# Optimization experiments

Measured on AMD Instinct MI355X. Metric: run time of the kernel, lower is better.

Reference implementation:

```python
import jax, jax.numpy as jnp
import numpy as np

K = 6  # knn_number
EPS_CS = 1e-8  # F.cosine_similarity eps


def _sqdist(a, b):
    # a: [B,N,3], b: [B,M,3] -> [B,N,M] squared euclidean distances
    return (jnp.sum(a * a, -1)[:, :, None]
            + jnp.sum(b * b, -1)[:, None, :]
            - 2.0 * jnp.einsum('bnc,bmc->bnm', a, b))


def _batch_norm(x):
    # normalize last dim with the module's exact epsilons
    n = jnp.sqrt(jnp.sum(x * x, axis=-1, keepdims=True) + 1e-08)
    return x / (n + 1e-10)


def _cossim(a, b):
    # torch F.cosine_similarity semantics along last dim
    na = jnp.maximum(jnp.sqrt(jnp.sum(a * a, -1)), EPS_CS)
    nb = jnp.maximum(jnp.sqrt(jnp.sum(b * b, -1)), EPS_CS)
    return jnp.sum(a * b, -1) / (na * nb)


def _gather(points, idx):
    # points: [B,N,C], idx: [B,...] int -> [B,...,C]
    return jax.vmap(lambda p, i: p[i])(points, idx)


def _avg_ori(group_ori, group_nor, batch_ori, batch_nor):
    # group_*: [B,N,K,3], batch_*: [B,N,3]
    nor_diff = jnp.sum(group_nor * batch_nor[:, :, None, :], axis=3)  # [B,N,K]
    nor_diff = jnp.exp(-nor_diff / 0.3) * 10.0 + 1.0
    nor_diff = jnp.where(nor_diff < 4.0, 1.0, 5.0)
    batch_ori_rot = jnp.cross(batch_ori, batch_nor)  # get_ori_rot90: ori x nor
    cos0 = _cossim(group_ori, batch_ori[:, :, None, :])       # [B,N,K]
    cos1 = _cossim(group_ori, batch_ori_rot[:, :, None, :])   # [B,N,K]
    cos = jnp.minimum(1.0 - jnp.abs(cos0), 1.0 - jnp.abs(cos1))
    return jnp.mean(nor_diff * cos)


def _forward(ori_pre, nor_pre, xyz_up, xyz_offset, pts, gt):
    ori_pre = _batch_norm(ori_pre)
    nor_pre = _batch_norm(nor_pre)
    xyz_gt = gt[:, :, 0:3]
    xyz_nor = gt[:, :, 3:6]

    # ori-loss: NN of pts in gt, gather gt normals
    index = jnp.argmin(_sqdist(pts, xyz_gt), axis=2)  # [B,N]
    nor_gt = _gather(xyz_nor, index)                  # [B,N,3]
    d_n = jnp.sum(nor_gt * ori_pre, axis=2, keepdims=True)
    ori_pro = _batch_norm(ori_pre - nor_gt * d_n)

    # smooth field over KNN (self-knn over pts, includes self)
    idx = jax.lax.top_k(-_sqdist(pts, pts), K)[1]  # [B,N,K]
    group_ori = _gather(ori_pro, idx)              # [B,N,K,3]
    group_nor = _gather(nor_gt, idx)
    loss_smooth = _avg_ori(group_ori, group_nor, ori_pro, nor_gt)

    # normal estimation loss
    loss_nor = jnp.mean(1.0 - jnp.abs(_cossim(nor_gt, nor_pre)))

    # chamfer distances (squared-dist chamfer)
    do = _sqdist(xyz_offset, xyz_gt)
    loss_charm_offset = jnp.mean(jnp.min(do, axis=2)) + jnp.mean(jnp.min(do, axis=1))
    du = _sqdist(xyz_up, xyz_gt)
    loss_charm = jnp.mean(jnp.min(du, axis=2)) + jnp.mean(jnp.min(du, axis=1))

    # nor-ori orthogonality
    loss_nor_ori = jnp.mean(jnp.abs(jnp.sum(ori_pre * nor_gt, axis=2)))

    loss_cd = loss_charm + 0.4 * loss_charm_offset
    loss = loss_smooth + loss_nor + 0.1 * loss_nor_ori + 200.0 * loss_cd
    return (loss, loss_smooth, loss_nor, loss_charm_offset, loss_nor_ori, loss_charm, loss_charm)


def setup_inputs() -> dict:
    key = jax.random.key(0)
    k = jax.random.split(key, 6)
    B, N, NG, NU = 4, 4096, 4096, 8192
    gt_xyz = jax.random.normal(k[5], (B, NG, 3), dtype=jnp.float32)
    gt_nor = _batch_norm(jax.random.normal(jax.random.fold_in(key, 7), (B, NG, 3), dtype=jnp.float32))
    return {
        'ori_pre': jax.random.normal(k[0], (B, N, 3), dtype=jnp.float32),
        'nor_pre': jax.random.normal(k[1], (B, N, 3), dtype=jnp.float32),
        'xyz_up': jax.random.normal(k[2], (B, NU, 3), dtype=jnp.float32),
        'xyz_offset': jax.random.normal(k[3], (B, NU, 3), dtype=jnp.float32),
        'pts': jax.random.normal(k[4], (B, N, 3), dtype=jnp.float32),
        'gt': jnp.concatenate([gt_xyz, gt_nor], axis=-1),
        'epoch': 1,
    }


def reference(ori_pre, nor_pre, xyz_up, xyz_offset, pts, gt, epoch):
    # epoch is unused by the original forward as well
    return _forward(ori_pre, nor_pre, xyz_up, xyz_offset, pts, gt)
```

## Files before the change

kernel.cpp:

```cpp
#include <hip/hip_runtime.h>
#include <stdint.h>

#define NN 4096
#define NGG 4096
#define NUU 8192

__device__ __forceinline__ unsigned fkey32(float f) {
  unsigned u = __float_as_uint(f);
  return u ^ (((int)u >> 31) | 0x80000000u);
}
__device__ __forceinline__ float unfkey32(unsigned k) {
  unsigned m = (k & 0x80000000u) ? 0x80000000u : 0xFFFFFFFFu;
  return __uint_as_float(k ^ m);
}

__device__ __forceinline__ float block_sum_256(float v, float* sbuf) {
#pragma unroll
  for (int o = 32; o > 0; o >>= 1) v += __shfl_down(v, o, 64);
  int lane = threadIdx.x & 63;
  int w = threadIdx.x >> 6;
  if (lane == 0) sbuf[w] = v;
  __syncthreads();
  float r = 0.f;
  if (threadIdx.x == 0) r = sbuf[0] + sbuf[1] + sbuf[2] + sbuf[3];
  __syncthreads();
  return r;
}

__device__ __forceinline__ float block_sum_512(float v, float* sbuf) {
#pragma unroll
  for (int o = 32; o > 0; o >>= 1) v += __shfl_down(v, o, 64);
  int lane = threadIdx.x & 63;
  int w = threadIdx.x >> 6;
  if (lane == 0) sbuf[w] = v;
  __syncthreads();
  float r = 0.f;
  if (threadIdx.x == 0) {
#pragma unroll
    for (int i = 0; i < 8; ++i) r += sbuf[i];
  }
  __syncthreads();
  return r;
}

__global__ __launch_bounds__(256) void k_scan(const float* __restrict__ pts,
                                              const float* __restrict__ gt,
                                              const float* __restrict__ up,
                                              const float* __restrict__ off,
                                              unsigned long long* __restrict__ keys,
                                              unsigned* __restrict__ rowmin,
                                              unsigned* __restrict__ colmin,
                                              float* __restrict__ acc) {
  __shared__ float4 sc[512];
  int blk = blockIdx.x;
  int tid = threadIdx.x;
  if (blk == 0 && tid < 16) acc[tid] = 0.f;

  if (blk < 512) {
    int qb = blk >> 3;
    int seg = blk & 7;
    int wb = qb >> 3;
    int which = wb >> 2;
    int b = wb & 3;
    int r0 = (qb & 7) * 1024 + tid * 4;
    {
      const float* gtb = gt + (size_t)b * NGG * 6 + (size_t)seg * 512 * 6;
      int i0 = tid * 2;
      const float4* g4 = (const float4*)(gtb + (size_t)i0 * 6);
      float4 u0 = g4[0], u1 = g4[1], u2 = g4[2];
      sc[i0] = make_float4(u0.x, u0.y, u0.z,
                           fmaf(u0.x, u0.x, fmaf(u0.y, u0.y, u0.z * u0.z)));
      sc[i0 + 1] = make_float4(u1.z, u1.w, u2.x,
                               fmaf(u1.z, u1.z, fmaf(u1.w, u1.w, u2.x * u2.x)));
    }
    const float* src = which ? up : off;
    const float4* s4 = (const float4*)src;
    size_t fb = ((size_t)(b * NUU + r0) * 3) >> 2;
    float4 A = s4[fb], B = s4[fb + 1], C = s4[fb + 2];
    float q0x = A.x, q0y = A.y, q0z = A.z;
    float q1x = A.w, q1y = B.x, q1z = B.y;
    float q2x = B.z, q2y = B.w, q2z = C.x;
    float q3x = C.y, q3y = C.z, q3z = C.w;
    float qq0 = fmaf(q0x, q0x, fmaf(q0y, q0y, q0z * q0z));
    float qq1 = fmaf(q1x, q1x, fmaf(q1y, q1y, q1z * q1z));
    float qq2 = fmaf(q2x, q2x, fmaf(q2y, q2y, q2z * q2z));
    float qq3 = fmaf(q3x, q3x, fmaf(q3y, q3y, q3z * q3z));
    float a0x = -2.f * q0x, a0y = -2.f * q0y, a0z = -2.f * q0z;
    float a1x = -2.f * q1x, a1y = -2.f * q1y, a1z = -2.f * q1z;
    float a2x = -2.f * q2x, a2y = -2.f * q2y, a2z = -2.f * q2z;
    float a3x = -2.f * q3x, a3y = -2.f * q3y, a3z = -2.f * q3z;
    __syncthreads();
    float b0 = 3.4e38f, b1 = 3.4e38f, b2 = 3.4e38f, b3 = 3.4e38f;
#pragma unroll 4
    for (int j = 0; j < 512; ++j) {
      float4 c = sc[j];
      float t;
      t = fmaf(c.x, a0x, c.w); t = fmaf(c.y, a0y, t); t = fmaf(c.z, a0z, t); b0 = fminf(b0, t);
      t = fmaf(c.x, a1x, c.w); t = fmaf(c.y, a1y, t); t = fmaf(c.z, a1z, t); b1 = fminf(b1, t);
      t = fmaf(c.x, a2x, c.w); t = fmaf(c.y, a2y, t); t = fmaf(c.z, a2z, t); b2 = fminf(b2, t);
      t = fmaf(c.x, a3x, c.w); t = fmaf(c.y, a3y, t); t = fmaf(c.z, a3z, t); b3 = fminf(b3, t);
    }
    int gr = which * 32768 + b * NUU + r0;
    atomicMin(&rowmin[gr + 0], fkey32(b0 + qq0));
    atomicMin(&rowmin[gr + 1], fkey32(b1 + qq1));
    atomicMin(&rowmin[gr + 2], fkey32(b2 + qq2));
    atomicMin(&rowmin[gr + 3], fkey32(b3 + qq3));

  } else if (blk < 1024) {
    int blk2 = blk - 512;
    int qb = blk2 >> 4;
    int seg = blk2 & 15;
    int which = qb >> 4;
    int b = (qb >> 2) & 3;
    int m0 = (qb & 3) * 1024 + tid * 4;
    const float* src = which ? up : off;
    if (tid < 128) {
      const float* sb = src + (size_t)b * NUU * 3 + (size_t)seg * 512 * 3;
      int i0 = tid * 4;
      const float4* s4 = (const float4*)(sb + (size_t)i0 * 3);
      float4 u0 = s4[0], u1 = s4[1], u2 = s4[2];
      sc[i0] = make_float4(u0.x, u0.y, u0.z,
                           fmaf(u0.x, u0.x, fmaf(u0.y, u0.y, u0.z * u0.z)));
      sc[i0 + 1] = make_float4(u0.w, u1.x, u1.y,
                               fmaf(u0.w, u0.w, fmaf(u1.x, u1.x, u1.y * u1.y)));
      sc[i0 + 2] = make_float4(u1.z, u1.w, u2.x,
                               fmaf(u1.z, u1.z, fmaf(u1.w, u1.w, u2.x * u2.x)));
      sc[i0 + 3] = make_float4(u2.y, u2.z, u2.w,
                               fmaf(u2.y, u2.y, fmaf(u2.z, u2.z, u2.w * u2.w)));
    }
    const float* g = gt + (size_t)b * NGG * 6 + (size_t)m0 * 6;
    float q0x = g[0],  q0y = g[1],  q0z = g[2];
    float q1x = g[6],  q1y = g[7],  q1z = g[8];
    float q2x = g[12], q2y = g[13], q2z = g[14];
    float q3x = g[18], q3y = g[19], q3z = g[20];
    float qq0 = fmaf(q0x, q0x, fmaf(q0y, q0y, q0z * q0z));
    float qq1 = fmaf(q1x, q1x, fmaf(q1y, q1y, q1z * q1z));
    float qq2 = fmaf(q2x, q2x, fmaf(q2y, q2y, q2z * q2z));
    float qq3 = fmaf(q3x, q3x, fmaf(q3y, q3y, q3z * q3z));
    float a0x = -2.f * q0x, a0y = -2.f * q0y, a0z = -2.f * q0z;
    float a1x = -2.f * q1x, a1y = -2.f * q1y, a1z = -2.f * q1z;
    float a2x = -2.f * q2x, a2y = -2.f * q2y, a2z = -2.f * q2z;
    float a3x = -2.f * q3x, a3y = -2.f * q3y, a3z = -2.f * q3z;
    __syncthreads();
    float b0 = 3.4e38f, b1 = 3.4e38f, b2 = 3.4e38f, b3 = 3.4e38f;
#pragma unroll 4
    for (int j = 0; j < 512; ++j) {
      float4 c = sc[j];
      float t;
      t = fmaf(c.x, a0x, c.w); t = fmaf(c.y, a0y, t); t = fmaf(c.z, a0z, t); b0 = fminf(b0, t);
      t = fmaf(c.x, a1x, c.w); t = fmaf(c.y, a1y, t); t = fmaf(c.z, a1z, t); b1 = fminf(b1, t);
      t = fmaf(c.x, a2x, c.w); t = fmaf(c.y, a2y, t); t = fmaf(c.z, a2z, t); b2 = fminf(b2, t);
      t = fmaf(c.x, a3x, c.w); t = fmaf(c.y, a3y, t); t = fmaf(c.z, a3z, t); b3 = fminf(b3, t);
    }
    int gc = which * 16384 + b * NGG + m0;
    atomicMin(&colmin[gc + 0], fkey32(b0 + qq0));
    atomicMin(&colmin[gc + 1], fkey32(b1 + qq1));
    atomicMin(&colmin[gc + 2], fkey32(b2 + qq2));
    atomicMin(&colmin[gc + 3], fkey32(b3 + qq3));

  } else {
    int blk3 = blk - 1024;
    int qb = blk3 >> 4;
    int seg = blk3 & 15;
    int b = qb >> 2;
    int m0 = (qb & 3) * 1024 + tid * 4;
    if (tid < 128) {
      const float* gtb = gt + (size_t)b * NGG * 6 + (size_t)seg * 256 * 6;
      int i0 = tid * 2;
      const float4* g4 = (const float4*)(gtb + (size_t)i0 * 6);
      float4 u0 = g4[0], u1 = g4[1], u2 = g4[2];
      sc[i0] = make_float4(u0.x, u0.y, u0.z,
                           fmaf(u0.x, u0.x, fmaf(u0.y, u0.y, u0.z * u0.z)));
      sc[i0 + 1] = make_float4(u1.z, u1.w, u2.x,
                               fmaf(u1.z, u1.z, fmaf(u1.w, u1.w, u2.x * u2.x)));
    }
    size_t fb = ((size_t)(b * NN + m0) * 3) >> 2;
    const float4* p4 = (const float4*)pts;
    float4 A = p4[fb], B = p4[fb + 1], C = p4[fb + 2];
    float q0x = A.x, q0y = A.y, q0z = A.z;
    float q1x = A.w, q1y = B.x, q1z = B.y;
    float q2x = B.z, q2y = B.w, q2z = C.x;
    float q3x = C.y, q3y = C.z, q3z = C.w;
    float a0x = -2.f * q0x, a0y = -2.f * q0y, a0z = -2.f * q0z;
    float a1x = -2.f * q1x, a1y = -2.f * q1y, a1z = -2.f * q1z;
    float a2x = -2.f * q2x, a2y = -2.f * q2y, a2z = -2.f * q2z;
    float a3x = -2.f * q3x, a3y = -2.f * q3y, a3z = -2.f * q3z;
    __syncthreads();
    float b0 = 3.4e38f, b1 = 3.4e38f, b2 = 3.4e38f, b3 = 3.4e38f;
    int i0 = 0, i1 = 0, i2 = 0, i3 = 0;
#pragma unroll 4
    for (int j = 0; j < 256; ++j) {
      float4 c = sc[j];
      float t; bool cc;
      t = fmaf(c.x, a0x, c.w); t = fmaf(c.y, a0y, t); t = fmaf(c.z, a0z, t);
      cc = t < b0; b0 = cc ? t : b0; i0 = cc ? j : i0;
      t = fmaf(c.x, a1x, c.w); t = fmaf(c.y, a1y, t); t = fmaf(c.z, a1z, t);
      cc = t < b1; b1 = cc ? t : b1; i1 = cc ? j : i1;
      t = fmaf(c.x, a2x, c.w); t = fmaf(c.y, a2y, t); t = fmaf(c.z, a2z, t);
      cc = t < b2; b2 = cc ? t : b2; i2 = cc ? j : i2;
      t = fmaf(c.x, a3x, c.w); t = fmaf(c.y, a3y, t); t = fmaf(c.z, a3z, t);
      cc = t < b3; b3 = cc ? t : b3; i3 = cc ? j : i3;
    }
    int q = b * NN + m0;
    int base = seg * 256;
    atomicMin(&keys[q + 0], ((unsigned long long)fkey32(b0) << 32) | (unsigned)(base + i0));
    atomicMin(&keys[q + 1], ((unsigned long long)fkey32(b1) << 32) | (unsigned)(base + i1));
    atomicMin(&keys[q + 2], ((unsigned long long)fkey32(b2) << 32) | (unsigned)(base + i2));
    atomicMin(&keys[q + 3], ((unsigned long long)fkey32(b3) << 32) | (unsigned)(base + i3));
  }
}

__global__ __launch_bounds__(256) void k_post(
    const float* __restrict__ ori_pre, const float* __restrict__ nor_pre,
    const float* __restrict__ gt, const unsigned long long* __restrict__ keys,
    const unsigned* __restrict__ rowmin, const unsigned* __restrict__ colmin,
    float* __restrict__ nor_gt, float* __restrict__ ori_pro, float* __restrict__ acc) {
  __shared__ float sb1[4], sb2[4];
  int blk = blockIdx.x;
  if (blk < 64) {
    int q = blk * 256 + threadIdx.x;
    int b = q >> 12;
    float ox = ori_pre[q * 3 + 0], oy = ori_pre[q * 3 + 1], oz = ori_pre[q * 3 + 2];
    float n1 = sqrtf(fmaf(ox, ox, fmaf(oy, oy, oz * oz)) + 1e-8f) + 1e-10f;
    ox /= n1; oy /= n1; oz /= n1;
    float px = nor_pre[q * 3 + 0], py = nor_pre[q * 3 + 1], pz = nor_pre[q * 3 + 2];
    float n2 = sqrtf(fmaf(px, px, fmaf(py, py, pz * pz)) + 1e-8f) + 1e-10f;
    px /= n2; py /= n2; pz /= n2;
    unsigned idx = (unsigned)(keys[q] & 0xffffffffULL);
    const float* g = gt + (size_t)b * NGG * 6 + (size_t)idx * 6 + 3;
    float gx = g[0], gy = g[1], gz = g[2];
    float dn = fmaf(gx, ox, fmaf(gy, oy, gz * oz));
    float vx = ox - gx * dn, vy = oy - gy * dn, vz = oz - gz * dn;
    float n3 = sqrtf(fmaf(vx, vx, fmaf(vy, vy, vz * vz)) + 1e-8f) + 1e-10f;
    vx /= n3; vy /= n3; vz /= n3;
    nor_gt[q * 3 + 0] = gx; nor_gt[q * 3 + 1] = gy; nor_gt[q * 3 + 2] = gz;
    ori_pro[q * 3 + 0] = vx; ori_pro[q * 3 + 1] = vy; ori_pro[q * 3 + 2] = vz;
    float na = fmaxf(sqrtf(fmaf(gx, gx, fmaf(gy, gy, gz * gz))), 1e-8f);
    float nb = fmaxf(sqrtf(fmaf(px, px, fmaf(py, py, pz * pz))), 1e-8f);
    float cs = fmaf(gx, px, fmaf(gy, py, gz * pz)) / (na * nb);
    float t_nor = 1.f - fabsf(cs);
    float t_ori = fabsf(dn);
    float s1 = block_sum_256(t_nor, sb1);
    float s2 = block_sum_256(t_ori, sb2);
    if (threadIdx.x == 0) {
      atomicAdd(&acc[1], s1);
      atomicAdd(&acc[2], s2);
    }
  } else {
    int rblk = blk - 64;
    float v;
    int slot;
    if (rblk < 256) {
      int i = rblk * 256 + threadIdx.x;
      v = unfkey32(rowmin[i]);
      slot = (i >> 15) ? 5 : 3;
    } else {
      int i = (rblk - 256) * 256 + threadIdx.x;
      v = unfkey32(colmin[i]);
      slot = (i >> 14) ? 6 : 4;
    }
    float s = block_sum_256(v, sb1);
    if (threadIdx.x == 0) atomicAdd(&acc[slot], s);
  }
}

#define EV(i, QX, QY, QZ) \
  fmaf(c##i##z, (QZ), fmaf(c##i##y, (QY), fmaf(c##i##x, (QX), c##i##w)))

#define MIN8Q(QX, QY, QZ) \
  fminf(fminf(fminf(EV(0, QX, QY, QZ), EV(1, QX, QY, QZ)),                    \
              fminf(EV(2, QX, QY, QZ), EV(3, QX, QY, QZ))),                   \
        fminf(fminf(EV(4, QX, QY, QZ), EV(5, QX, QY, QZ)),                    \
              fminf(EV(6, QX, QY, QZ), EV(7, QX, QY, QZ))))

#define WREDMIN(M)                                            \
  {                                                           \
    M = fminf(M, __shfl_xor(M, 32, 64));                      \
    M = fminf(M, __shfl_xor(M, 16, 64));                      \
    M = fminf(M, __shfl_xor(M, 8, 64));                       \
    M = fminf(M, __shfl_xor(M, 4, 64));                       \
    M = fminf(M, __shfl_xor(M, 2, 64));                       \
    M = fminf(M, __shfl_xor(M, 1, 64));                       \
  }

#define PUSH1(QI, E, IDX)                                                     \
  if ((E) <= tq) {                                                            \
    unsigned sl = atomicAdd(&scnt[QI], 1u);                                   \
    if (sl < 96)                                                              \
      surv[QI][sl] = ((unsigned long long)fkey32(E) << 32) | (unsigned)(IDX); \
  }

#define PASSB_Q(QI, QX, QY, QZ)                                               \
  {                                                                           \
    float tq = stau[QI];                                                      \
    float e0 = EV(0, QX, QY, QZ), e1 = EV(1, QX, QY, QZ);                     \
    float e2 = EV(2, QX, QY, QZ), e3 = EV(3, QX, QY, QZ);                     \
    float e4 = EV(4, QX, QY, QZ), e5 = EV(5, QX, QY, QZ);                     \
    float e6 = EV(6, QX, QY, QZ), e7 = EV(7, QX, QY, QZ);                     \
    float mm = fminf(fminf(fminf(e0, e1), fminf(e2, e3)),                     \
                     fminf(fminf(e4, e5), fminf(e6, e7)));                    \
    if (mm <= tq) {                                                           \
      int base = tid * 8;                                                     \
      PUSH1(QI, e0, base + 0) PUSH1(QI, e1, base + 1)                         \
      PUSH1(QI, e2, base + 2) PUSH1(QI, e3, base + 3)                         \
      PUSH1(QI, e4, base + 4) PUSH1(QI, e5, base + 5)                         \
      PUSH1(QI, e6, base + 6) PUSH1(QI, e7, base + 7)                         \
    }                                                                         \
  }

#define TAUC(VI)                                                              \
  {                                                                           \
    int nct = (v0 <= (VI)) + (v1 <= (VI)) + (v2 <= (VI)) + (v3 <= (VI)) +     \
              (v4 <= (VI)) + (v5 <= (VI)) + (v6 <= (VI)) + (v7 <= (VI));      \
    if (nct >= 6) tau = fminf(tau, (VI));                                     \
  }

__global__ __launch_bounds__(512, 4) void k_knn_smooth(const float* __restrict__ pts,
                                                       const float* __restrict__ nor_gt,
                                                       const float* __restrict__ ori_pro,
                                                       float* __restrict__ acc,
                                                       float* __restrict__ out) {
  __shared__ unsigned long long surv[16][96];
  __shared__ unsigned scnt[16];
  __shared__ float wmin[8][16];
  __shared__ float stau[16];
  __shared__ float sred[8];
  int tid = threadIdx.x;
  int lane = tid & 63;
  int wave = tid >> 6;
  int blk = blockIdx.x;
  int b = blk >> 8;
  const float* pb = pts + (size_t)b * NN * 3;
  const float* pq = pb + (size_t)((blk & 255) * 16) * 3;

  if (tid < 16) scnt[tid] = 0;

  float c0x, c0y, c0z, c0w, c1x, c1y, c1z, c1w, c2x, c2y, c2z, c2w,
      c3x, c3y, c3z, c3w, c4x, c4y, c4z, c4w, c5x, c5y, c5z, c5w,
      c6x, c6y, c6z, c6w, c7x, c7y, c7z, c7w;
  {
    const float4* p4 = (const float4*)(pb + (size_t)tid * 24);
    float4 u0 = p4[0], u1 = p4[1], u2 = p4[2], u3 = p4[3], u4 = p4[4], u5 = p4[5];
    c0x = u0.x; c0y = u0.y; c0z = u0.z;
    c1x = u0.w; c1y = u1.x; c1z = u1.y;
    c2x = u1.z; c2y = u1.w; c2z = u2.x;
    c3x = u2.y; c3y = u2.z; c3z = u2.w;
    c4x = u3.x; c4y = u3.y; c4z = u3.z;
    c5x = u3.w; c5y = u4.x; c5z = u4.y;
    c6x = u4.z; c6y = u4.w; c6z = u5.x;
    c7x = u5.y; c7y = u5.z; c7z = u5.w;
    c0w = fmaf(c0x, c0x, fmaf(c0y, c0y, c0z * c0z));
    c1w = fmaf(c1x, c1x, fmaf(c1y, c1y, c1z * c1z));
    c2w = fmaf(c2x, c2x, fmaf(c2y, c2y, c2z * c2z));
    c3w = fmaf(c3x, c3x, fmaf(c3y, c3y, c3z * c3z));
    c4w = fmaf(c4x, c4x, fmaf(c4y, c4y, c4z * c4z));
    c5w = fmaf(c5x, c5x, fmaf(c5y, c5y, c5z * c5z));
    c6w = fmaf(c6x, c6x, fmaf(c6y, c6y, c6z * c6z));
    c7w = fmaf(c7x, c7x, fmaf(c7y, c7y, c7z * c7z));
  }

  for (int ch = 0; ch < 4; ++ch) {
    const float* qp = pq + ch * 12;
    float Q0x = -2.f * qp[0],  Q0y = -2.f * qp[1],  Q0z = -2.f * qp[2];
    float Q1x = -2.f * qp[3],  Q1y = -2.f * qp[4],  Q1z = -2.f * qp[5];
    float Q2x = -2.f * qp[6],  Q2y = -2.f * qp[7],  Q2z = -2.f * qp[8];
    float Q3x = -2.f * qp[9],  Q3y = -2.f * qp[10], Q3z = -2.f * qp[11];
    float m0 = MIN8Q(Q0x, Q0y, Q0z);
    float m1 = MIN8Q(Q1x, Q1y, Q1z);
    float m2 = MIN8Q(Q2x, Q2y, Q2z);
    float m3 = MIN8Q(Q3x, Q3y, Q3z);
    WREDMIN(m0) WREDMIN(m1) WREDMIN(m2) WREDMIN(m3)
    if (lane == 0) {
      wmin[wave][ch * 4 + 0] = m0;
      wmin[wave][ch * 4 + 1] = m1;
      wmin[wave][ch * 4 + 2] = m2;
      wmin[wave][ch * 4 + 3] = m3;
    }
  }
  __syncthreads();

  if (tid < 16) {
    float v0 = wmin[0][tid], v1 = wmin[1][tid], v2 = wmin[2][tid],
          v3 = wmin[3][tid], v4 = wmin[4][tid], v5 = wmin[5][tid],
          v6 = wmin[6][tid], v7 = wmin[7][tid];
    float tau = 3.4e38f;
    TAUC(v0) TAUC(v1) TAUC(v2) TAUC(v3) TAUC(v4) TAUC(v5) TAUC(v6) TAUC(v7)
    stau[tid] = tau;
  }
  __syncthreads();

  for (int ch = 0; ch < 4; ++ch) {
    const float* qp = pq + ch * 12;
    float Q0x = -2.f * qp[0],  Q0y = -2.f * qp[1],  Q0z = -2.f * qp[2];
    float Q1x = -2.f * qp[3],  Q1y = -2.f * qp[4],  Q1z = -2.f * qp[5];
    float Q2x = -2.f * qp[6],  Q2y = -2.f * qp[7],  Q2z = -2.f * qp[8];
    float Q3x = -2.f * qp[9],  Q3y = -2.f * qp[10], Q3z = -2.f * qp[11];
    PASSB_Q(ch * 4 + 0, Q0x, Q0y, Q0z)
    PASSB_Q(ch * 4 + 1, Q1x, Q1y, Q1z)
    PASSB_Q(ch * 4 + 2, Q2x, Q2y, Q2z)
    PASSB_Q(ch * 4 + 3, Q3x, Q3y, Q3z)
  }
  __syncthreads();

  int q_local = tid >> 5;
  int t = tid & 31;
  int q = blk * 16 + q_local;
  unsigned cnt = scnt[q_local];
  if (cnt > 96) cnt = 96;
  unsigned long long l0 = ~0ULL, l1 = ~0ULL, l2 = ~0ULL;
  for (int i = t; i < (int)cnt; i += 32) {
    unsigned long long k = surv[q_local][i];
    bool cc; unsigned long long nk;
    cc = k < l0; nk = cc ? k : l0; k = cc ? l0 : k; l0 = nk;
    cc = k < l1; nk = cc ? k : l1; k = cc ? l1 : k; l1 = nk;
    cc = k < l2; nk = cc ? k : l2;                  l2 = nk;
  }
  int myid = 0;
#pragma unroll
  for (int r = 0; r < 6; ++r) {
    unsigned long long h = l0, mk = l0;
#pragma unroll
    for (int o = 16; o > 0; o >>= 1) {
      unsigned long long other = __shfl_xor(mk, o, 32);
      mk = (other < mk) ? other : mk;
    }
    if (t == r) myid = (int)(mk & 0xffffffffULL);
    if (h == mk) { l0 = l1; l1 = l2; l2 = ~0ULL; }
  }

  float sum = 0.f;
  if (t < 6) {
    const float* gq = nor_gt + (size_t)q * 3;
    float ngx = gq[0], ngy = gq[1], ngz = gq[2];
    const float* oq = ori_pro + (size_t)q * 3;
    float box = oq[0], boy = oq[1], boz = oq[2];
    float rx = boy * ngz - boz * ngy;
    float ry = boz * ngx - box * ngz;
    float rz = box * ngy - boy * ngx;
    float nbo = fmaxf(sqrtf(fmaf(box, box, fmaf(boy, boy, boz * boz))), 1e-8f);
    float nrot = fmaxf(sqrtf(fmaf(rx, rx, fmaf(ry, ry, rz * rz))), 1e-8f);
    const float* gn = nor_gt + (size_t)(b * 4096 + myid) * 3;
    const float* go = ori_pro + (size_t)(b * 4096 + myid) * 3;
    float gnx = gn[0], gny = gn[1], gnz = gn[2];
    float gox = go[0], goy = go[1], goz = go[2];
    float ndv = fmaf(gnx, ngx, fmaf(gny, ngy, gnz * ngz));
    float wv = (expf(-ndv / 0.3f) * 10.f + 1.f) < 4.f ? 1.f : 5.f;
    float ngo = fmaxf(sqrtf(fmaf(gox, gox, fmaf(goy, goy, goz * goz))), 1e-8f);
    float c0 = fmaf(gox, box, fmaf(goy, boy, goz * boz)) / (ngo * nbo);
    float c1 = fmaf(gox, rx, fmaf(goy, ry, goz * rz)) / (ngo * nrot);
    float cosv = fminf(1.f - fabsf(c0), 1.f - fabsf(c1));
    sum = wv * cosv;
  }
  float s = block_sum_512(sum, sred);

  if (tid == 0) {
    atomicAdd(&acc[0], s);
    __threadfence();
    unsigned c = atomicAdd((unsigned*)(acc + 9), 1u);
    if (c == gridDim.x - 1) {
      __threadfence();
      float a0 = atomicAdd(&acc[0], 0.f);
      float a1 = atomicAdd(&acc[1], 0.f);
      float a2 = atomicAdd(&acc[2], 0.f);
      float a3 = atomicAdd(&acc[3], 0.f);
      float a4 = atomicAdd(&acc[4], 0.f);
      float a5 = atomicAdd(&acc[5], 0.f);
      float a6 = atomicAdd(&acc[6], 0.f);
      float loss_smooth = a0 / 98304.f;
      float loss_nor = a1 / 16384.f;
      float loss_nor_ori = a2 / 16384.f;
      float lco = a3 / 32768.f + a4 / 16384.f;
      float lc = a5 / 32768.f + a6 / 16384.f;
      float loss_cd = lc + 0.4f * lco;
      float loss = loss_smooth + loss_nor + 0.1f * loss_nor_ori + 200.f * loss_cd;
      out[0] = loss;
      out[1] = loss_smooth;
      out[2] = loss_nor;
      out[3] = lco;
      out[4] = loss_nor_ori;
      out[5] = lc;
      out[6] = lc;
    }
  }
}

extern "C" void kernel_launch(void* const* d_in, const int* in_sizes, int n_in,
                              void* d_out, int out_size, void* d_ws, size_t ws_size,
                              hipStream_t stream) {
  (void)in_sizes; (void)n_in; (void)out_size; (void)ws_size;
  const float* ori_pre = (const float*)d_in[0];
  const float* nor_pre = (const float*)d_in[1];
  const float* xyz_up = (const float*)d_in[2];
  const float* xyz_off = (const float*)d_in[3];
  const float* pts = (const float*)d_in[4];
  const float* gt = (const float*)d_in[5];
  float* out = (float*)d_out;
  char* ws = (char*)d_ws;

  float* acc = (float*)(ws + 0);
  unsigned long long* keys = (unsigned long long*)(ws + 512);
  unsigned* rowmin = (unsigned*)(ws + 512 + 131072);
  unsigned* colmin = (unsigned*)(ws + 512 + 131072 + 262144);
  float* nor_gt = (float*)(ws + 512 + 131072 + 262144 + 131072);
  float* ori_pro = (float*)(ws + 512 + 131072 + 262144 + 131072 + 196608);

  hipMemsetAsync(ws + 512, 0xFF, 131072 + 262144 + 131072, stream);

  k_scan<<<1280, 256, 0, stream>>>(pts, gt, xyz_up, xyz_off, keys, rowmin,
                                   colmin, acc);
  k_post<<<448, 256, 0, stream>>>(ori_pre, nor_pre, gt, keys, rowmin, colmin,
                                  nor_gt, ori_pro, acc);
  k_knn_smooth<<<1024, 512, 0, stream>>>(pts, nor_gt, ori_pro, acc, out);
}
```

Baseline: 170.5 us.

## Fuse post-processing kernel into KNN smooth kernel, recomputing projected orientations on the fly

Removes the k_post launch and the nor_gt/ori_pro intermediate buffers. The KNN smooth kernel now recomputes the projected orientation and the gathered GT normal for each query and neighbor from keys, gt and ori_pre. The row/col min reductions and the per-point normal losses move into extra blocks of the same grid. This saves one kernel launch and a global round trip, at the cost of redundant recomputation (about 6 neighbor projections per query) with extra dependent gathers.

```diff
diff --git a/kernel.cpp b/kernel.cpp
--- a/kernel.cpp
+++ b/kernel.cpp
@@ -12,19 +12,6 @@
 __device__ __forceinline__ float unfkey32(unsigned k) {
   unsigned m = (k & 0x80000000u) ? 0x80000000u : 0xFFFFFFFFu;
   return __uint_as_float(k ^ m);
-}
-
-__device__ __forceinline__ float block_sum_256(float v, float* sbuf) {
-#pragma unroll
-  for (int o = 32; o > 0; o >>= 1) v += __shfl_down(v, o, 64);
-  int lane = threadIdx.x & 63;
-  int w = threadIdx.x >> 6;
-  if (lane == 0) sbuf[w] = v;
-  __syncthreads();
-  float r = 0.f;
-  if (threadIdx.x == 0) r = sbuf[0] + sbuf[1] + sbuf[2] + sbuf[3];
-  __syncthreads();
-  return r;
 }
 
 __device__ __forceinline__ float block_sum_512(float v, float* sbuf) {
@@ -210,59 +197,22 @@
   }
 }
 
-__global__ __launch_bounds__(256) void k_post(
-    const float* __restrict__ ori_pre, const float* __restrict__ nor_pre,
-    const float* __restrict__ gt, const unsigned long long* __restrict__ keys,
-    const unsigned* __restrict__ rowmin, const unsigned* __restrict__ colmin,
-    float* __restrict__ nor_gt, float* __restrict__ ori_pro, float* __restrict__ acc) {
-  __shared__ float sb1[4], sb2[4];
-  int blk = blockIdx.x;
-  if (blk < 64) {
-    int q = blk * 256 + threadIdx.x;
-    int b = q >> 12;
-    float ox = ori_pre[q * 3 + 0], oy = ori_pre[q * 3 + 1], oz = ori_pre[q * 3 + 2];
-    float n1 = sqrtf(fmaf(ox, ox, fmaf(oy, oy, oz * oz)) + 1e-8f) + 1e-10f;
-    ox /= n1; oy /= n1; oz /= n1;
-    float px = nor_pre[q * 3 + 0], py = nor_pre[q * 3 + 1], pz = nor_pre[q * 3 + 2];
-    float n2 = sqrtf(fmaf(px, px, fmaf(py, py, pz * pz)) + 1e-8f) + 1e-10f;
-    px /= n2; py /= n2; pz /= n2;
-    unsigned idx = (unsigned)(keys[q] & 0xffffffffULL);
-    const float* g = gt + (size_t)b * NGG * 6 + (size_t)idx * 6 + 3;
-    float gx = g[0], gy = g[1], gz = g[2];
-    float dn = fmaf(gx, ox, fmaf(gy, oy, gz * oz));
-    float vx = ox - gx * dn, vy = oy - gy * dn, vz = oz - gz * dn;
-    float n3 = sqrtf(fmaf(vx, vx, fmaf(vy, vy, vz * vz)) + 1e-8f) + 1e-10f;
-    vx /= n3; vy /= n3; vz /= n3;
-    nor_gt[q * 3 + 0] = gx; nor_gt[q * 3 + 1] = gy; nor_gt[q * 3 + 2] = gz;
-    ori_pro[q * 3 + 0] = vx; ori_pro[q * 3 + 1] = vy; ori_pro[q * 3 + 2] = vz;
-    float na = fmaxf(sqrtf(fmaf(gx, gx, fmaf(gy, gy, gz * gz))), 1e-8f);
-    float nb = fmaxf(sqrtf(fmaf(px, px, fmaf(py, py, pz * pz))), 1e-8f);
-    float cs = fmaf(gx, px, fmaf(gy, py, gz * pz)) / (na * nb);
-    float t_nor = 1.f - fabsf(cs);
-    float t_ori = fabsf(dn);
-    float s1 = block_sum_256(t_nor, sb1);
-    float s2 = block_sum_256(t_ori, sb2);
-    if (threadIdx.x == 0) {
-      atomicAdd(&acc[1], s1);
-      atomicAdd(&acc[2], s2);
-    }
-  } else {
-    int rblk = blk - 64;
-    float v;
-    int slot;
-    if (rblk < 256) {
-      int i = rblk * 256 + threadIdx.x;
-      v = unfkey32(rowmin[i]);
-      slot = (i >> 15) ? 5 : 3;
-    } else {
-      int i = (rblk - 256) * 256 + threadIdx.x;
-      v = unfkey32(colmin[i]);
-      slot = (i >> 14) ? 6 : 4;
-    }
-    float s = block_sum_256(v, sb1);
-    if (threadIdx.x == 0) atomicAdd(&acc[slot], s);
-  }
-}
+#define PROJ_ORI(GIDX, NGX, NGY, NGZ, BOX, BOY, BOZ)                          \
+  {                                                                           \
+    unsigned idq_ = (unsigned)(keys[GIDX] & 0xffffffffULL);                   \
+    const float* g_ = gt + (size_t)b * NGG * 6 + (size_t)idq_ * 6 + 3;        \
+    NGX = g_[0]; NGY = g_[1]; NGZ = g_[2];                                    \
+    float ox_ = ori_pre[(GIDX) * 3 + 0], oy_ = ori_pre[(GIDX) * 3 + 1],       \
+          oz_ = ori_pre[(GIDX) * 3 + 2];                                      \
+    float n1_ = sqrtf(fmaf(ox_, ox_, fmaf(oy_, oy_, oz_ * oz_)) + 1e-8f) +    \
+                1e-10f;                                                       \
+    ox_ /= n1_; oy_ /= n1_; oz_ /= n1_;                                       \
+    float dn_ = fmaf(NGX, ox_, fmaf(NGY, oy_, NGZ * oz_));                    \
+    float vx_ = ox_ - NGX * dn_, vy_ = oy_ - NGY * dn_, vz_ = oz_ - NGZ * dn_;\
+    float n3_ = sqrtf(fmaf(vx_, vx_, fmaf(vy_, vy_, vz_ * vz_)) + 1e-8f) +    \
+                1e-10f;                                                       \
+    BOX = vx_ / n3_; BOY = vy_ / n3_; BOZ = vz_ / n3_;                        \
+  }
 
 #define EV(i, QX, QY, QZ) \
   fmaf(c##i##z, (QZ), fmaf(c##i##y, (QY), fmaf(c##i##x, (QX), c##i##w)))
@@ -279,7 +229,7 @@
     M = fminf(M, __shfl_xor(M, 16, 64));                      \
     M = fminf(M, __shfl_xor(M, 8, 64));                       \
     M = fminf(M, __shfl_xor(M, 4, 64));                       \
-    M = fminf(M, __shfl_xor(M, 2, 64));                       \
+    M = fminf(M, __shfl_xor(M, 2, 64));                      \
     M = fminf(M, __shfl_xor(M, 1, 64));                       \
   }
 
@@ -315,146 +265,187 @@
     if (nct >= 6) tau = fminf(tau, (VI));                                     \
   }
 
-__global__ __launch_bounds__(512, 4) void k_knn_smooth(const float* __restrict__ pts,
-                                                       const float* __restrict__ nor_gt,
-                                                       const float* __restrict__ ori_pro,
-                                                       float* __restrict__ acc,
-                                                       float* __restrict__ out) {
+__global__ __launch_bounds__(512, 4) void k_final(const float* __restrict__ pts,
+                                                  const float* __restrict__ gt,
+                                                  const float* __restrict__ ori_pre,
+                                                  const float* __restrict__ nor_pre,
+                                                  const unsigned* __restrict__ rowmin,
+                                                  const unsigned* __restrict__ colmin,
+                                                  const unsigned long long* __restrict__ keys,
+                                                  float* __restrict__ acc,
+                                                  float* __restrict__ out) {
   __shared__ unsigned long long surv[16][96];
   __shared__ unsigned scnt[16];
   __shared__ float wmin[8][16];
   __shared__ float stau[16];
   __shared__ float sred[8];
   int tid = threadIdx.x;
-  int lane = tid & 63;
-  int wave = tid >> 6;
   int blk = blockIdx.x;
-  int b = blk >> 8;
-  const float* pb = pts + (size_t)b * NN * 3;
-  const float* pq = pb + (size_t)((blk & 255) * 16) * 3;
-
-  if (tid < 16) scnt[tid] = 0;
-
-  float c0x, c0y, c0z, c0w, c1x, c1y, c1z, c1w, c2x, c2y, c2z, c2w,
-      c3x, c3y, c3z, c3w, c4x, c4y, c4z, c4w, c5x, c5y, c5z, c5w,
-      c6x, c6y, c6z, c6w, c7x, c7y, c7z, c7w;
-  {
-    const float4* p4 = (const float4*)(pb + (size_t)tid * 24);
-    float4 u0 = p4[0], u1 = p4[1], u2 = p4[2], u3 = p4[3], u4 = p4[4], u5 = p4[5];
-    c0x = u0.x; c0y = u0.y; c0z = u0.z;
-    c1x = u0.w; c1y = u1.x; c1z = u1.y;
-    c2x = u1.z; c2y = u1.w; c2z = u2.x;
-    c3x = u2.y; c3y = u2.z; c3z = u2.w;
-    c4x = u3.x; c4y = u3.y; c4z = u3.z;
-    c5x = u3.w; c5y = u4.x; c5z = u4.y;
-    c6x = u4.z; c6y = u4.w; c6z = u5.x;
-    c7x = u5.y; c7y = u5.z; c7z = u5.w;
-    c0w = fmaf(c0x, c0x, fmaf(c0y, c0y, c0z * c0z));
-    c1w = fmaf(c1x, c1x, fmaf(c1y, c1y, c1z * c1z));
-    c2w = fmaf(c2x, c2x, fmaf(c2y, c2y, c2z * c2z));
-    c3w = fmaf(c3x, c3x, fmaf(c3y, c3y, c3z * c3z));
-    c4w = fmaf(c4x, c4x, fmaf(c4y, c4y, c4z * c4z));
-    c5w = fmaf(c5x, c5x, fmaf(c5y, c5y, c5z * c5z));
-    c6w = fmaf(c6x, c6x, fmaf(c6y, c6y, c6z * c6z));
-    c7w = fmaf(c7x, c7x, fmaf(c7y, c7y, c7z * c7z));
-  }
-
-  for (int ch = 0; ch < 4; ++ch) {
-    const float* qp = pq + ch * 12;
-    float Q0x = -2.f * qp[0],  Q0y = -2.f * qp[1],  Q0z = -2.f * qp[2];
-    float Q1x = -2.f * qp[3],  Q1y = -2.f * qp[4],  Q1z = -2.f * qp[5];
-    float Q2x = -2.f * qp[6],  Q2y = -2.f * qp[7],  Q2z = -2.f * qp[8];
-    float Q3x = -2.f * qp[9],  Q3y = -2.f * qp[10], Q3z = -2.f * qp[11];
-    float m0 = MIN8Q(Q0x, Q0y, Q0z);
-    float m1 = MIN8Q(Q1x, Q1y, Q1z);
-    float m2 = MIN8Q(Q2x, Q2y, Q2z);
-    float m3 = MIN8Q(Q3x, Q3y, Q3z);
-    WREDMIN(m0) WREDMIN(m1) WREDMIN(m2) WREDMIN(m3)
-    if (lane == 0) {
-      wmin[wave][ch * 4 + 0] = m0;
-      wmin[wave][ch * 4 + 1] = m1;
-      wmin[wave][ch * 4 + 2] = m2;
-      wmin[wave][ch * 4 + 3] = m3;
-    }
-  }
-  __syncthreads();
-
-  if (tid < 16) {
-    float v0 = wmin[0][tid], v1 = wmin[1][tid], v2 = wmin[2][tid],
-          v3 = wmin[3][tid], v4 = wmin[4][tid], v5 = wmin[5][tid],
-          v6 = wmin[6][tid], v7 = wmin[7][tid];
-    float tau = 3.4e38f;
-    TAUC(v0) TAUC(v1) TAUC(v2) TAUC(v3) TAUC(v4) TAUC(v5) TAUC(v6) TAUC(v7)
-    stau[tid] = tau;
-  }
-  __syncthreads();
-
-  for (int ch = 0; ch < 4; ++ch) {
-    const float* qp = pq + ch * 12;
-    float Q0x = -2.f * qp[0],  Q0y = -2.f * qp[1],  Q0z = -2.f * qp[2];
-    float Q1x = -2.f * qp[3],  Q1y = -2.f * qp[4],  Q1z = -2.f * qp[5];
-    float Q2x = -2.f * qp[6],  Q2y = -2.f * qp[7],  Q2z = -2.f * qp[8];
-    float Q3x = -2.f * qp[9],  Q3y = -2.f * qp[10], Q3z = -2.f * qp[11];
-    PASSB_Q(ch * 4 + 0, Q0x, Q0y, Q0z)
-    PASSB_Q(ch * 4 + 1, Q1x, Q1y, Q1z)
-    PASSB_Q(ch * 4 + 2, Q2x, Q2y, Q2z)
-    PASSB_Q(ch * 4 + 3, Q3x, Q3y, Q3z)
-  }
-  __syncthreads();
-
-  int q_local = tid >> 5;
-  int t = tid & 31;
-  int q = blk * 16 + q_local;
-  unsigned cnt = scnt[q_local];
-  if (cnt > 96) cnt = 96;
-  unsigned long long l0 = ~0ULL, l1 = ~0ULL, l2 = ~0ULL;
-  for (int i = t; i < (int)cnt; i += 32) {
-    unsigned long long k = surv[q_local][i];
-    bool cc; unsigned long long nk;
-    cc = k < l0; nk = cc ? k : l0; k = cc ? l0 : k; l0 = nk;
-    cc = k < l1; nk = cc ? k : l1; k = cc ? l1 : k; l1 = nk;
-    cc = k < l2; nk = cc ? k : l2;                  l2 = nk;
-  }
-  int myid = 0;
+
+  if (blk < 1024) {
+    int lane = tid & 63;
+    int wave = tid >> 6;
+    int b = blk >> 8;
+    const float* pb = pts + (size_t)b * NN * 3;
+    const float* pq = pb + (size_t)((blk & 255) * 16) * 3;
+
+    if (tid < 16) scnt[tid] = 0;
+
+    float c0x, c0y, c0z, c0w, c1x, c1y, c1z, c1w, c2x, c2y, c2z, c2w,
+        c3x, c3y, c3z, c3w, c4x, c4y, c4z, c4w, c5x, c5y, c5z, c5w,
+        c6x, c6y, c6z, c6w, c7x, c7y, c7z, c7w;
+    {
+      const float4* p4 = (const float4*)(pb + (size_t)tid * 24);
+      float4 u0 = p4[0], u1 = p4[1], u2 = p4[2], u3 = p4[3], u4 = p4[4], u5 = p4[5];
+      c0x = u0.x; c0y = u0.y; c0z = u0.z;
+      c1x = u0.w; c1y = u1.x; c1z = u1.y;
+      c2x = u1.z; c2y = u1.w; c2z = u2.x;
+      c3x = u2.y; c3y = u2.z; c3z = u2.w;
+      c4x = u3.x; c4y = u3.y; c4z = u3.z;
+      c5x = u3.w; c5y = u4.x; c5z = u4.y;
+      c6x = u4.z; c6y = u4.w; c6z = u5.x;
+      c7x = u5.y; c7y = u5.z; c7z = u5.w;
+      c0w = fmaf(c0x, c0x, fmaf(c0y, c0y, c0z * c0z));
+      c1w = fmaf(c1x, c1x, fmaf(c1y, c1y, c1z * c1z));
+      c2w = fmaf(c2x, c2x, fmaf(c2y, c2y, c2z * c2z));
+      c3w = fmaf(c3x, c3x, fmaf(c3y, c3y, c3z * c3z));
+      c4w = fmaf(c4x, c4x, fmaf(c4y, c4y, c4z * c4z));
+      c5w = fmaf(c5x, c5x, fmaf(c5y, c5y, c5z * c5z));
+      c6w = fmaf(c6x, c6x, fmaf(c6y, c6y, c6z * c6z));
+      c7w = fmaf(c7x, c7x, fmaf(c7y, c7y, c7z * c7z));
+    }
+
+    for (int ch = 0; ch < 4; ++ch) {
+      const float* qp = pq + ch * 12;
+      float Q0x = -2.f * qp[0],  Q0y = -2.f * qp[1],  Q0z = -2.f * qp[2];
+      float Q1x = -2.f * qp[3],  Q1y = -2.f * qp[4],  Q1z = -2.f * qp[5];
+      float Q2x = -2.f * qp[6],  Q2y = -2.f * qp[7],  Q2z = -2.f * qp[8];
+      float Q3x = -2.f * qp[9],  Q3y = -2.f * qp[10], Q3z = -2.f * qp[11];
+      float m0 = MIN8Q(Q0x, Q0y, Q0z);
+      float m1 = MIN8Q(Q1x, Q1y, Q1z);
+      float m2 = MIN8Q(Q2x, Q2y, Q2z);
+      float m3 = MIN8Q(Q3x, Q3y, Q3z);
+      WREDMIN(m0) WREDMIN(m1) WREDMIN(m2) WREDMIN(m3)
+      if (lane == 0) {
+        wmin[wave][ch * 4 + 0] = m0;
+        wmin[wave][ch * 4 + 1] = m1;
+        wmin[wave][ch * 4 + 2] = m2;
+        wmin[wave][ch * 4 + 3] = m3;
+      }
+    }
+    __syncthreads();
+
+    if (tid < 16) {
+      float v0 = wmin[0][tid], v1 = wmin[1][tid], v2 = wmin[2][tid],
+            v3 = wmin[3][tid], v4 = wmin[4][tid], v5 = wmin[5][tid],
+            v6 = wmin[6][tid], v7 = wmin[7][tid];
+      float tau = 3.4e38f;
+      TAUC(v0) TAUC(v1) TAUC(v2) TAUC(v3) TAUC(v4) TAUC(v5) TAUC(v6) TAUC(v7)
+      stau[tid] = tau;
+    }
+    __syncthreads();
+
+    for (int ch = 0; ch < 4; ++ch) {
+      const float* qp = pq + ch * 12;
+      float Q0x = -2.f * qp[0],  Q0y = -2.f * qp[1],  Q0z = -2.f * qp[2];
+      float Q1x = -2.f * qp[3],  Q1y = -2.f * qp[4],  Q1z = -2.f * qp[5];
+      float Q2x = -2.f * qp[6],  Q2y = -2.f * qp[7],  Q2z = -2.f * qp[8];
+      float Q3x = -2.f * qp[9],  Q3y = -2.f * qp[10], Q3z = -2.f * qp[11];
+      PASSB_Q(ch * 4 + 0, Q0x, Q0y, Q0z)
+      PASSB_Q(ch * 4 + 1, Q1x, Q1y, Q1z)
+      PASSB_Q(ch * 4 + 2, Q2x, Q2y, Q2z)
+      PASSB_Q(ch * 4 + 3, Q3x, Q3y, Q3z)
+    }
+    __syncthreads();
+
+    int q_local = tid >> 5;
+    int t = tid & 31;
+    int q = blk * 16 + q_local;
+    unsigned cnt = scnt[q_local];
+    if (cnt > 96) cnt = 96;
+    unsigned long long l0 = ~0ULL, l1 = ~0ULL, l2 = ~0ULL;
+    for (int i = t; i < (int)cnt; i += 32) {
+      unsigned long long k = surv[q_local][i];
+      bool cc; unsigned long long nk;
+      cc = k < l0; nk = cc ? k : l0; k = cc ? l0 : k; l0 = nk;
+      cc = k < l1; nk = cc ? k : l1; k = cc ? l1 : k; l1 = nk;
+      cc = k < l2; nk = cc ? k : l2;                  l2 = nk;
+    }
+    int myid = 0;
 #pragma unroll
-  for (int r = 0; r < 6; ++r) {
-    unsigned long long h = l0, mk = l0;
+    for (int r = 0; r < 6; ++r) {
+      unsigned long long h = l0, mk = l0;
 #pragma unroll
-    for (int o = 16; o > 0; o >>= 1) {
-      unsigned long long other = __shfl_xor(mk, o, 32);
-      mk = (other < mk) ? other : mk;
-    }
-    if (t == r) myid = (int)(mk & 0xffffffffULL);
-    if (h == mk) { l0 = l1; l1 = l2; l2 = ~0ULL; }
-  }
-
-  float sum = 0.f;
-  if (t < 6) {
-    const float* gq = nor_gt + (size_t)q * 3;
-    float ngx = gq[0], ngy = gq[1], ngz = gq[2];
-    const float* oq = ori_pro + (size_t)q * 3;
-    float box = oq[0], boy = oq[1], boz = oq[2];
-    float rx = boy * ngz - boz * ngy;
-    float ry = boz * ngx - box * ngz;
-    float rz = box * ngy - boy * ngx;
-    float nbo = fmaxf(sqrtf(fmaf(box, box, fmaf(boy, boy, boz * boz))), 1e-8f);
-    float nrot = fmaxf(sqrtf(fmaf(rx, rx, fmaf(ry, ry, rz * rz))), 1e-8f);
-    const float* gn = nor_gt + (size_t)(b * 4096 + myid) * 3;
-    const float* go = ori_pro + (size_t)(b * 4096 + myid) * 3;
-    float gnx = gn[0], gny = gn[1], gnz = gn[2];
-    float gox = go[0], goy = go[1], goz = go[2];
-    float ndv = fmaf(gnx, ngx, fmaf(gny, ngy, gnz * ngz));
-    float wv = (expf(-ndv / 0.3f) * 10.f + 1.f) < 4.f ? 1.f : 5.f;
-    float ngo = fmaxf(sqrtf(fmaf(gox, gox, fmaf(goy, goy, goz * goz))), 1e-8f);
-    float c0 = fmaf(gox, box, fmaf(goy, boy, goz * boz)) / (ngo * nbo);
-    float c1 = fmaf(gox, rx, fmaf(goy, ry, goz * rz)) / (ngo * nrot);
-    float cosv = fminf(1.f - fabsf(c0), 1.f - fabsf(c1));
-    sum = wv * cosv;
-  }
-  float s = block_sum_512(sum, sred);
+      for (int o = 16; o > 0; o >>= 1) {
+        unsigned long long other = __shfl_xor(mk, o, 32);
+        mk = (other < mk) ? other : mk;
+      }
+      if (t == r) myid = (int)(mk & 0xffffffffULL);
+      if (h == mk) { l0 = l1; l1 = l2; l2 = ~0ULL; }
+    }
+
+    float sum = 0.f;
+    if (t < 6) {
+      float ngx, ngy, ngz, box, boy, boz;
+      PROJ_ORI(q, ngx, ngy, ngz, box, boy, boz)
+      int nb = b * 4096 + myid;
+      float gnx, gny, gnz, gox, goy, goz;
+      PROJ_ORI(nb, gnx, gny, gnz, gox, goy, goz)
+      float rx = boy * ngz - boz * ngy;
+      float ry = boz * ngx - box * ngz;
+      float rz = box * ngy - boy * ngx;
+      float nbo = fmaxf(sqrtf(fmaf(box, box, fmaf(boy, boy, boz * boz))), 1e-8f);
+      float nrot = fmaxf(sqrtf(fmaf(rx, rx, fmaf(ry, ry, rz * rz))), 1e-8f);
+      float ndv = fmaf(gnx, ngx, fmaf(gny, ngy, gnz * ngz));
+      float wv = (expf(-ndv / 0.3f) * 10.f + 1.f) < 4.f ? 1.f : 5.f;
+      float ngo = fmaxf(sqrtf(fmaf(gox, gox, fmaf(goy, goy, goz * goz))), 1e-8f);
+      float c0 = fmaf(gox, box, fmaf(goy, boy, goz * boz)) / (ngo * nbo);
+      float c1 = fmaf(gox, rx, fmaf(goy, ry, goz * rz)) / (ngo * nrot);
+      float cosv = fminf(1.f - fabsf(c0), 1.f - fabsf(c1));
+      sum = wv * cosv;
+    }
+    float s = block_sum_512(sum, sred);
+    if (tid == 0) atomicAdd(&acc[0], s);
+
+  } else if (blk < 1152) {
+    int i = (blk - 1024) * 512 + tid;
+    float v = unfkey32(rowmin[i]);
+    int slot = (i >> 15) ? 5 : 3;
+    float s = block_sum_512(v, sred);
+    if (tid == 0) atomicAdd(&acc[slot], s);
+  } else if (blk < 1216) {
+    int i = (blk - 1152) * 512 + tid;
+    float v = unfkey32(colmin[i]);
+    int slot = (i >> 14) ? 6 : 4;
+    float s = block_sum_512(v, sred);
+    if (tid == 0) atomicAdd(&acc[slot], s);
+  } else {
+    int q = (blk - 1216) * 512 + tid;
+    int b = q >> 12;
+    float ox = ori_pre[q * 3 + 0], oy = ori_pre[q * 3 + 1], oz = ori_pre[q * 3 + 2];
+    float n1 = sqrtf(fmaf(ox, ox, fmaf(oy, oy, oz * oz)) + 1e-8f) + 1e-10f;
+    ox /= n1; oy /= n1; oz /= n1;
+    float px = nor_pre[q * 3 + 0], py = nor_pre[q * 3 + 1], pz = nor_pre[q * 3 + 2];
+    float n2 = sqrtf(fmaf(px, px, fmaf(py, py, pz * pz)) + 1e-8f) + 1e-10f;
+    px /= n2; py /= n2; pz /= n2;
+    unsigned idx = (unsigned)(keys[q] & 0xffffffffULL);
+    const float* g = gt + (size_t)b * NGG * 6 + (size_t)idx * 6 + 3;
+    float gx = g[0], gy = g[1], gz = g[2];
+    float dn = fmaf(gx, ox, fmaf(gy, oy, gz * oz));
+    float na = fmaxf(sqrtf(fmaf(gx, gx, fmaf(gy, gy, gz * gz))), 1e-8f);
+    float nb = fmaxf(sqrtf(fmaf(px, px, fmaf(py, py, pz * pz))), 1e-8f);
+    float cs = fmaf(gx, px, fmaf(gy, py, gz * pz)) / (na * nb);
+    float t_nor = 1.f - fabsf(cs);
+    float t_ori = fabsf(dn);
+    float s1 = block_sum_512(t_nor, sred);
+    float s2 = block_sum_512(t_ori, sred);
+    if (tid == 0) {
+      atomicAdd(&acc[1], s1);
+      atomicAdd(&acc[2], s2);
+    }
+  }
 
   if (tid == 0) {
-    atomicAdd(&acc[0], s);
     __threadfence();
     unsigned c = atomicAdd((unsigned*)(acc + 9), 1u);
     if (c == gridDim.x - 1) {
@@ -501,14 +492,11 @@
   unsigned long long* keys = (unsigned long long*)(ws + 512);
   unsigned* rowmin = (unsigned*)(ws + 512 + 131072);
   unsigned* colmin = (unsigned*)(ws + 512 + 131072 + 262144);
-  float* nor_gt = (float*)(ws + 512 + 131072 + 262144 + 131072);
-  float* ori_pro = (float*)(ws + 512 + 131072 + 262144 + 131072 + 196608);
 
   hipMemsetAsync(ws + 512, 0xFF, 131072 + 262144 + 131072, stream);
 
   k_scan<<<1280, 256, 0, stream>>>(pts, gt, xyz_up, xyz_off, keys, rowmin,
                                    colmin, acc);
-  k_post<<<448, 256, 0, stream>>>(ori_pre, nor_pre, gt, keys, rowmin, colmin,
-                                  nor_gt, ori_pro, acc);
-  k_knn_smooth<<<1024, 512, 0, stream>>>(pts, nor_gt, ori_pro, acc, out);
+  k_final<<<1248, 512, 0, stream>>>(pts, gt, ori_pre, nor_pre, rowmin, colmin,
+                                    keys, acc, out);
 }
```

New measurement: 171.8 us. No clear change (+0.8%).
